# Performance work log

Measured on AMD Instinct MI355X. Metric: run time of the kernel, lower is better.

The kernel has to match this reference:

```python
import jax, jax.numpy as jnp
import numpy as np

B, P, K = 32, 1024, 16  # clouds, points per cloud, neighbors


def setup_inputs() -> dict:
    key = jax.random.key(0)
    ks = jax.random.split(key, 5)
    N, C, H, D = B * P, 64, 128, 3
    x = jax.random.normal(ks[0], (N, C), dtype=jnp.float32)
    pos = jax.random.normal(ks[1], (N, D), dtype=jnp.float32)
    batch = jnp.arange(N, dtype=jnp.int64) // P  # cloud id per node
    W_e = jax.random.normal(ks[2], (2 * C, H), dtype=jnp.float32) * 0.05
    b_e = jnp.zeros((H,), dtype=jnp.float32)
    W_sc = jax.random.normal(ks[3], (C, H), dtype=jnp.float32) * 0.05
    b_sc = jnp.zeros((H,), dtype=jnp.float32)
    return {"x": x, "pos": pos, "batch": batch,
            "W_e": W_e, "b_e": b_e, "W_sc": W_sc, "b_sc": b_sc}


def _knn_idx(posb):
    # posb: [B, P, D] -> idx [B, P, K]: K nearest neighbors (sources) per target node,
    # within each cloud, excluding self (loop=False in torch_geometric.knn_graph).
    sq = jnp.sum(posb * posb, axis=-1)                       # [B, P]
    d2 = sq[:, :, None] + sq[:, None, :] - 2.0 * jnp.einsum('bid,bjd->bij', posb, posb)
    d2 = d2 + jnp.eye(P, dtype=posb.dtype)[None] * jnp.finfo(posb.dtype).max / 2
    _, idx = jax.lax.top_k(-d2, K)                           # [B, P, K]
    return idx


def reference(x, pos, batch, W_e, b_e, W_sc, b_sc):
    C = x.shape[-1]
    xb = x.reshape(B, P, C)
    posb = pos.reshape(B, P, -1)
    idx = _knn_idx(posb)                                     # [B, P, K]
    # gather neighbor (source) features per target node
    x_j = jax.vmap(lambda xc, ic: xc[ic])(xb, idx)           # [B, P, K, C]
    x_i = xb[:, :, None, :]                                  # [B, P, 1, C]
    # EdgeConv message: nn([x_i, x_j - x_i]), here Linear + ReLU
    e = jnp.concatenate([jnp.broadcast_to(x_i, x_j.shape), x_j - x_i], axis=-1)  # [B,P,K,2C]
    msg = jax.nn.relu(jnp.einsum('bpke,eh->bpkh', e, W_e) + b_e)
    agg = jnp.max(msg, axis=2)                               # max aggregation -> [B, P, H]
    shortcut = x @ W_sc + b_sc                               # [N, H]
    out = agg.reshape(-1, agg.shape[-1]) + shortcut
    return out
```

## Files before the change

kernel.cpp:

```cpp
#include <hip/hip_runtime.h>
#include <float.h>
#include <stdint.h>

#define BATCHES 32
#define P 1024
#define KNN 16
#define C 64
#define H 128
#define N (BATCHES * P)
#define NCOLS 384
#define SPLITS 8
#define CPS 128
#define PADH 132

typedef short short8 __attribute__((ext_vector_type(8)));
typedef float floatx4 __attribute__((ext_vector_type(4)));

__device__ __forceinline__ unsigned short f2bf(float f) {
    unsigned u = __float_as_uint(f);
    unsigned r = (u + 0x7FFF + ((u >> 16) & 1)) >> 16;
    return (unsigned short)r;
}

__global__ __launch_bounds__(256) void prep_w(
    const float* __restrict__ W_e, const float* __restrict__ b_e,
    const float* __restrict__ W_sc, const float* __restrict__ b_sc,
    unsigned short* __restrict__ WT, float* __restrict__ bias)
{
    int i = blockIdx.x * 256 + threadIdx.x;
    int col = i >> 6, c = i & 63;
    float w;
    if (col < 128)      w = W_e[c * 128 + col] - W_e[(64 + c) * 128 + col];
    else if (col < 256) w = W_e[(64 + c) * 128 + (col - 128)];
    else                w = W_sc[c * 128 + (col - 256)];
    WT[col * 64 + c] = f2bf(w);
    if (c == 0) {
        bias[col] = (col < 128) ? b_e[col] : (col < 256 ? 0.0f : b_sc[col - 256]);
    }
}

struct alignas(16) F4 { float x, y, z, w; };

struct PA {
    F4    spos[P + 8];
    float lists[SPLITS][16][64];
    unsigned short offs[SPLITS][64];
    unsigned short cnts[SPLITS][64];
    float Tq[64];
};
struct PB {
    unsigned short Ubuf[64][PADH];
    unsigned short Vbuf[64][PADH];
    unsigned short Sbuf[64][PADH];
};

__global__ __launch_bounds__(512) void knn_gemm_kernel(
    const float* __restrict__ pos, const float* __restrict__ X,
    const unsigned short* __restrict__ WT, const float* __restrict__ bias,
    int* __restrict__ idx_out,
    unsigned short* __restrict__ U, unsigned short* __restrict__ V,
    unsigned short* __restrict__ S)
{
    __shared__ __align__(16) char smraw[sizeof(PA)];
    PA* A  = (PA*)smraw;
    PB* Bm = (PB*)smraw;

    int t = threadIdx.x;
    int q = t & 63, s = t >> 6;
    int blk = blockIdx.x;
    int batch = blk >> 4;
    int qblk  = blk & 15;
    int iloc  = qblk * 64 + q;

    const float* pb = pos + (size_t)batch * P * 3;
    for (int j = t; j < P; j += 512) {
        float x = pb[j * 3 + 0], y = pb[j * 3 + 1], z = pb[j * 3 + 2];
        float sq = __fadd_rn(__fadd_rn(__fmul_rn(x, x), __fmul_rn(y, y)),
                             __fmul_rn(z, z));
        A->spos[j] = F4{x, y, z, sq};
    }
    __syncthreads();

    F4 me = A->spos[iloc];
    const int j0 = s * CPS;

    float d[16];
#pragma unroll
    for (int k = 0; k < 16; ++k) d[k] = FLT_MAX;

    auto dist = [&](const F4& c, int j) -> float {
        float dot = __fadd_rn(__fadd_rn(__fmul_rn(me.x, c.x), __fmul_rn(me.y, c.y)),
                              __fmul_rn(me.z, c.z));
        float d2 = __fadd_rn(__fadd_rn(me.w, c.w), __fmul_rn(-2.0f, dot));
        return (j == iloc) ? FLT_MAX : d2;
    };
    auto insert = [&](float d2) {
#pragma unroll
        for (int k = 15; k >= 1; --k)
            d[k] = __builtin_amdgcn_fmed3f(d[k - 1], d2, d[k]);
        d[0] = fminf(d[0], d2);
    };

    {
        F4 c0 = A->spos[j0 + 0], c1 = A->spos[j0 + 1];
        F4 c2 = A->spos[j0 + 2], c3 = A->spos[j0 + 3];
#pragma unroll 2
        for (int jj = 0; jj < CPS; jj += 4) {
            F4 n0 = A->spos[j0 + jj + 4];
            F4 n1 = A->spos[j0 + jj + 5];
            F4 n2 = A->spos[j0 + jj + 6];
            F4 n3 = A->spos[j0 + jj + 7];
            insert(dist(c0, j0 + jj + 0));
            insert(dist(c1, j0 + jj + 1));
            insert(dist(c2, j0 + jj + 2));
            insert(dist(c3, j0 + jj + 3));
            c0 = n0; c1 = n1; c2 = n2; c3 = n3;
        }
    }
#pragma unroll
    for (int k = 0; k < 16; ++k) A->lists[s][k][q] = d[k];
    __syncthreads();

    if (s == 0) {
        float v0 = A->lists[0][0][q], v1 = A->lists[1][0][q];
        float v2 = A->lists[2][0][q], v3 = A->lists[3][0][q];
        float v4 = A->lists[4][0][q], v5 = A->lists[5][0][q];
        float v6 = A->lists[6][0][q], v7 = A->lists[7][0][q];
        float w0 = A->lists[0][1][q], w1 = A->lists[1][1][q];
        float w2 = A->lists[2][1][q], w3 = A->lists[3][1][q];
        float w4 = A->lists[4][1][q], w5 = A->lists[5][1][q];
        float w6 = A->lists[6][1][q], w7 = A->lists[7][1][q];
        int n0 = 0, n1 = 0, n2 = 0, n3 = 0, n4 = 0, n5 = 0, n6 = 0, n7 = 0;
        float T = 0.0f;
#pragma unroll 1
        for (int k = 0; k < 16; ++k) {
            float mn = fminf(fminf(fminf(v0, v1), fminf(v2, v3)),
                             fminf(fminf(v4, v5), fminf(v6, v7)));
            if      (v0 == mn) { n0++; v0 = w0; w0 = (n0 + 1 < 16) ? A->lists[0][n0 + 1][q] : FLT_MAX; }
            else if (v1 == mn) { n1++; v1 = w1; w1 = (n1 + 1 < 16) ? A->lists[1][n1 + 1][q] : FLT_MAX; }
            else if (v2 == mn) { n2++; v2 = w2; w2 = (n2 + 1 < 16) ? A->lists[2][n2 + 1][q] : FLT_MAX; }
            else if (v3 == mn) { n3++; v3 = w3; w3 = (n3 + 1 < 16) ? A->lists[3][n3 + 1][q] : FLT_MAX; }
            else if (v4 == mn) { n4++; v4 = w4; w4 = (n4 + 1 < 16) ? A->lists[4][n4 + 1][q] : FLT_MAX; }
            else if (v5 == mn) { n5++; v5 = w5; w5 = (n5 + 1 < 16) ? A->lists[5][n5 + 1][q] : FLT_MAX; }
            else if (v6 == mn) { n6++; v6 = w6; w6 = (n6 + 1 < 16) ? A->lists[6][n6 + 1][q] : FLT_MAX; }
            else               { n7++; v7 = w7; w7 = (n7 + 1 < 16) ? A->lists[7][n7 + 1][q] : FLT_MAX; }
            T = mn;
        }
        A->Tq[q] = T;
        int off = 0;
        A->offs[0][q] = (unsigned short)off; A->cnts[0][q] = (unsigned short)n0; off += n0;
        A->offs[1][q] = (unsigned short)off; A->cnts[1][q] = (unsigned short)n1; off += n1;
        A->offs[2][q] = (unsigned short)off; A->cnts[2][q] = (unsigned short)n2; off += n2;
        A->offs[3][q] = (unsigned short)off; A->cnts[3][q] = (unsigned short)n3; off += n3;
        A->offs[4][q] = (unsigned short)off; A->cnts[4][q] = (unsigned short)n4; off += n4;
        A->offs[5][q] = (unsigned short)off; A->cnts[5][q] = (unsigned short)n5; off += n5;
        A->offs[6][q] = (unsigned short)off; A->cnts[6][q] = (unsigned short)n6; off += n6;
        A->offs[7][q] = (unsigned short)off; A->cnts[7][q] = (unsigned short)n7;
    }
    __syncthreads();

    {
        float T  = A->Tq[q];
        int   cap = A->cnts[s][q];
        int   gb  = ((blk << 6) + q) * KNN + A->offs[s][q];
        int   base = batch * P;
        int   cnt = 0;

        F4 c0 = A->spos[j0 + 0], c1 = A->spos[j0 + 1];
        F4 c2 = A->spos[j0 + 2], c3 = A->spos[j0 + 3];
#pragma unroll 2
        for (int jj = 0; jj < CPS; jj += 4) {
            F4 n0 = A->spos[j0 + jj + 4];
            F4 n1 = A->spos[j0 + jj + 5];
            F4 n2 = A->spos[j0 + jj + 6];
            F4 n3 = A->spos[j0 + jj + 7];
#pragma unroll
            for (int u = 0; u < 4; ++u) {
                const F4& c = (u == 0) ? c0 : (u == 1) ? c1 : (u == 2) ? c2 : c3;
                int j = j0 + jj + u;
                float d2 = dist(c, j);
                if (d2 <= T && cnt < cap) {
                    idx_out[gb + cnt] = base + j;
                    cnt++;
                }
            }
            c0 = n0; c1 = n1; c2 = n2; c3 = n3;
        }
    }
    __syncthreads();

    {
        int mt = s & 3, nh = s >> 2;
        int m0 = blk * 64 + mt * 16;
        int lm = q & 15, kg = q >> 4;

        const float4* arow = (const float4*)(X + (size_t)(m0 + lm) * 64 + kg * 8);
        float4 f0 = arow[0], f1 = arow[1];
        float4 f2 = arow[8], f3 = arow[9];
        short8 a0, a1;
        a0[0] = (short)f2bf(f0.x); a0[1] = (short)f2bf(f0.y);
        a0[2] = (short)f2bf(f0.z); a0[3] = (short)f2bf(f0.w);
        a0[4] = (short)f2bf(f1.x); a0[5] = (short)f2bf(f1.y);
        a0[6] = (short)f2bf(f1.z); a0[7] = (short)f2bf(f1.w);
        a1[0] = (short)f2bf(f2.x); a1[1] = (short)f2bf(f2.y);
        a1[2] = (short)f2bf(f2.z); a1[3] = (short)f2bf(f2.w);
        a1[4] = (short)f2bf(f3.x); a1[5] = (short)f2bf(f3.y);
        a1[6] = (short)f2bf(f3.z); a1[7] = (short)f2bf(f3.w);

#pragma unroll 4
        for (int nt = nh * 12; nt < nh * 12 + 12; ++nt) {
            const short8* brow = (const short8*)(WT + (size_t)(nt * 16 + lm) * 64 + kg * 8);
            short8 b0 = brow[0];
            short8 b1 = brow[4];
            floatx4 acc = {0.0f, 0.0f, 0.0f, 0.0f};
            acc = __builtin_amdgcn_mfma_f32_16x16x32_bf16(a0, b0, acc, 0, 0, 0);
            acc = __builtin_amdgcn_mfma_f32_16x16x32_bf16(a1, b1, acc, 0, 0, 0);

            int col = nt * 16 + lm;
            float bv = bias[col];
#pragma unroll
            for (int r = 0; r < 4; ++r) {
                int row = mt * 16 + kg * 4 + r;
                unsigned short val = f2bf(acc[r] + bv);
                if (col < 128)      Bm->Ubuf[row][col] = val;
                else if (col < 256) Bm->Vbuf[row][col - 128] = val;
                else                Bm->Sbuf[row][col - 256] = val;
            }
        }
    }
    __syncthreads();

    {
        uint2* Ug = (uint2*)U + (size_t)blk * 2048;
        uint2* Vg = (uint2*)V + (size_t)blk * 2048;
        uint2* Sg = (uint2*)S + (size_t)blk * 2048;
#pragma unroll
        for (int i = t; i < 2048; i += 512) {
            int row = i >> 5, off = (i & 31) * 4;
            Ug[i] = *(const uint2*)&Bm->Ubuf[row][off];
            Vg[i] = *(const uint2*)&Bm->Vbuf[row][off];
            Sg[i] = *(const uint2*)&Bm->Sbuf[row][off];
        }
    }
}

__global__ __launch_bounds__(256) void final_kernel(
    const int* __restrict__ idx, const unsigned short* __restrict__ U,
    const unsigned short* __restrict__ V, const unsigned short* __restrict__ S,
    float* __restrict__ out)
{
    int t = threadIdx.x;
    __shared__ int nbr[8][KNN];
    if (t < 128) ((int*)nbr)[t] = idx[(size_t)blockIdx.x * 128 + t];
    __syncthreads();

    int w = t >> 6, l = t & 63;
    int half = l >> 5, c4 = l & 31;
    int pl = w * 2 + half;
    size_t p = (size_t)blockIdx.x * 8 + pl;

    uint2 uu = ((const uint2*)(U + p * H))[c4];
    uint2 ss = ((const uint2*)(S + p * H))[c4];

    float m0 = -FLT_MAX, m1 = -FLT_MAX, m2 = -FLT_MAX, m3 = -FLT_MAX;
#pragma unroll
    for (int k = 0; k < KNN; ++k) {
        int row = nbr[pl][k];
        uint2 vv = *(const uint2*)(V + (size_t)row * H + c4 * 4);
        m0 = fmaxf(m0, __uint_as_float(vv.x << 16));
        m1 = fmaxf(m1, __uint_as_float(vv.x & 0xFFFF0000u));
        m2 = fmaxf(m2, __uint_as_float(vv.y << 16));
        m3 = fmaxf(m3, __uint_as_float(vv.y & 0xFFFF0000u));
    }

    float4 o;
    o.x = fmaxf(__uint_as_float(uu.x << 16)          + m0, 0.0f) + __uint_as_float(ss.x << 16);
    o.y = fmaxf(__uint_as_float(uu.x & 0xFFFF0000u)  + m1, 0.0f) + __uint_as_float(ss.x & 0xFFFF0000u);
    o.z = fmaxf(__uint_as_float(uu.y << 16)          + m2, 0.0f) + __uint_as_float(ss.y << 16);
    o.w = fmaxf(__uint_as_float(uu.y & 0xFFFF0000u)  + m3, 0.0f) + __uint_as_float(ss.y & 0xFFFF0000u);
    ((float4*)(out + p * H))[c4] = o;
}

extern "C" void kernel_launch(void* const* d_in, const int* in_sizes, int n_in,
                              void* d_out, int out_size, void* d_ws, size_t ws_size,
                              hipStream_t stream)
{
    const float* x    = (const float*)d_in[0];
    const float* pos  = (const float*)d_in[1];
    const float* W_e  = (const float*)d_in[3];
    const float* b_e  = (const float*)d_in[4];
    const float* W_sc = (const float*)d_in[5];
    const float* b_sc = (const float*)d_in[6];
    float* out = (float*)d_out;

    char* ws = (char*)d_ws;
    const size_t OFF_IDX  = 0;
    const size_t OFF_U    = 2ull << 20;
    const size_t OFF_V    = OFF_U + (8ull << 20);
    const size_t OFF_S    = OFF_V + (8ull << 20);
    const size_t OFF_WT   = OFF_S + (8ull << 20);
    const size_t OFF_BIAS = OFF_WT + 49152;

    int*            idx  = (int*)(ws + OFF_IDX);
    unsigned short* U    = (unsigned short*)(ws + OFF_U);
    unsigned short* V    = (unsigned short*)(ws + OFF_V);
    unsigned short* S    = (unsigned short*)(ws + OFF_S);
    unsigned short* WT   = (unsigned short*)(ws + OFF_WT);
    float*          bias = (float*)(ws + OFF_BIAS);

    prep_w<<<(NCOLS * C) / 256, 256, 0, stream>>>(W_e, b_e, W_sc, b_sc, WT, bias);
    knn_gemm_kernel<<<512, 512, 0, stream>>>(pos, x, WT, bias, idx, U, V, S);
    final_kernel<<<N / 8, 256, 0, stream>>>(idx, U, V, S, out);
}
```

Baseline: 144.2 us.

## Precompute packed pos+norm in prep kernel; read candidates from global instead of LDS

The per-point packing of positions and squared norms moves into the prep kernel, which writes a float4 array to workspace. The kNN kernel no longer stages all 1024 points of its cloud into shared memory. It reads candidate positions directly from global memory, where they are wave-uniform and so can become scalar loads thanks to readfirstlane on the split index. This cuts the LDS footprint and removes a sync, which may raise occupancy, but it adds a global read path and an extra workspace buffer.

Measured after the change: 147.4 us. 2.2% more time.

```diff
diff --git a/kernel.cpp b/kernel.cpp
--- a/kernel.cpp
+++ b/kernel.cpp
@@ -22,27 +22,36 @@
     return (unsigned short)r;
 }
 
-__global__ __launch_bounds__(256) void prep_w(
+struct alignas(16) F4 { float x, y, z, w; };
+
+__global__ __launch_bounds__(256) void prep_kernel(
     const float* __restrict__ W_e, const float* __restrict__ b_e,
     const float* __restrict__ W_sc, const float* __restrict__ b_sc,
-    unsigned short* __restrict__ WT, float* __restrict__ bias)
-{
-    int i = blockIdx.x * 256 + threadIdx.x;
-    int col = i >> 6, c = i & 63;
-    float w;
-    if (col < 128)      w = W_e[c * 128 + col] - W_e[(64 + c) * 128 + col];
-    else if (col < 256) w = W_e[(64 + c) * 128 + (col - 128)];
-    else                w = W_sc[c * 128 + (col - 256)];
-    WT[col * 64 + c] = f2bf(w);
-    if (c == 0) {
-        bias[col] = (col < 128) ? b_e[col] : (col < 256 ? 0.0f : b_sc[col - 256]);
-    }
-}
-
-struct alignas(16) F4 { float x, y, z, w; };
+    const float* __restrict__ pos,
+    unsigned short* __restrict__ WT, float* __restrict__ bias,
+    F4* __restrict__ posq)
+{
+    int b = blockIdx.x;
+    if (b < 96) {
+        int i = b * 256 + threadIdx.x;
+        int col = i >> 6, c = i & 63;
+        float w;
+        if (col < 128)      w = W_e[c * 128 + col] - W_e[(64 + c) * 128 + col];
+        else if (col < 256) w = W_e[(64 + c) * 128 + (col - 128)];
+        else                w = W_sc[c * 128 + (col - 256)];
+        WT[col * 64 + c] = f2bf(w);
+        if (c == 0)
+            bias[col] = (col < 128) ? b_e[col] : (col < 256 ? 0.0f : b_sc[col - 256]);
+    } else {
+        int i = (b - 96) * 256 + threadIdx.x;
+        float x = pos[i * 3 + 0], y = pos[i * 3 + 1], z = pos[i * 3 + 2];
+        float sq = __fadd_rn(__fadd_rn(__fmul_rn(x, x), __fmul_rn(y, y)),
+                             __fmul_rn(z, z));
+        posq[i] = F4{x, y, z, sq};
+    }
+}
 
 struct PA {
-    F4    spos[P + 8];
     float lists[SPLITS][16][64];
     unsigned short offs[SPLITS][64];
     unsigned short cnts[SPLITS][64];
@@ -55,67 +64,48 @@
 };
 
 __global__ __launch_bounds__(512) void knn_gemm_kernel(
-    const float* __restrict__ pos, const float* __restrict__ X,
+    const F4* __restrict__ posq, const float* __restrict__ X,
     const unsigned short* __restrict__ WT, const float* __restrict__ bias,
     int* __restrict__ idx_out,
     unsigned short* __restrict__ U, unsigned short* __restrict__ V,
     unsigned short* __restrict__ S)
 {
-    __shared__ __align__(16) char smraw[sizeof(PA)];
+    __shared__ __align__(16) char smraw[sizeof(PB)];
     PA* A  = (PA*)smraw;
     PB* Bm = (PB*)smraw;
 
     int t = threadIdx.x;
-    int q = t & 63, s = t >> 6;
+    int q = t & 63;
+    int s = __builtin_amdgcn_readfirstlane(t >> 6);
     int blk = blockIdx.x;
     int batch = blk >> 4;
     int qblk  = blk & 15;
     int iloc  = qblk * 64 + q;
 
-    const float* pb = pos + (size_t)batch * P * 3;
-    for (int j = t; j < P; j += 512) {
-        float x = pb[j * 3 + 0], y = pb[j * 3 + 1], z = pb[j * 3 + 2];
-        float sq = __fadd_rn(__fadd_rn(__fmul_rn(x, x), __fmul_rn(y, y)),
-                             __fmul_rn(z, z));
-        A->spos[j] = F4{x, y, z, sq};
-    }
-    __syncthreads();
-
-    F4 me = A->spos[iloc];
+    const F4* __restrict__ pbq = posq + (size_t)batch * P;
     const int j0 = s * CPS;
-
-    float d[16];
-#pragma unroll
-    for (int k = 0; k < 16; ++k) d[k] = FLT_MAX;
-
-    auto dist = [&](const F4& c, int j) -> float {
+    const F4* __restrict__ pcand = pbq + j0;
+
+    F4 me = pbq[iloc];
+
+    auto dist = [&](F4 c, int j) -> float {
         float dot = __fadd_rn(__fadd_rn(__fmul_rn(me.x, c.x), __fmul_rn(me.y, c.y)),
                               __fmul_rn(me.z, c.z));
         float d2 = __fadd_rn(__fadd_rn(me.w, c.w), __fmul_rn(-2.0f, dot));
         return (j == iloc) ? FLT_MAX : d2;
     };
-    auto insert = [&](float d2) {
+
+    float d[16];
+#pragma unroll
+    for (int k = 0; k < 16; ++k) d[k] = FLT_MAX;
+
+#pragma unroll 8
+    for (int jj = 0; jj < CPS; ++jj) {
+        float d2 = dist(pcand[jj], j0 + jj);
 #pragma unroll
         for (int k = 15; k >= 1; --k)
             d[k] = __builtin_amdgcn_fmed3f(d[k - 1], d2, d[k]);
         d[0] = fminf(d[0], d2);
-    };
-
-    {
-        F4 c0 = A->spos[j0 + 0], c1 = A->spos[j0 + 1];
-        F4 c2 = A->spos[j0 + 2], c3 = A->spos[j0 + 3];
-#pragma unroll 2
-        for (int jj = 0; jj < CPS; jj += 4) {
-            F4 n0 = A->spos[j0 + jj + 4];
-            F4 n1 = A->spos[j0 + jj + 5];
-            F4 n2 = A->spos[j0 + jj + 6];
-            F4 n3 = A->spos[j0 + jj + 7];
-            insert(dist(c0, j0 + jj + 0));
-            insert(dist(c1, j0 + jj + 1));
-            insert(dist(c2, j0 + jj + 2));
-            insert(dist(c3, j0 + jj + 3));
-            c0 = n0; c1 = n1; c2 = n2; c3 = n3;
-        }
     }
 #pragma unroll
     for (int k = 0; k < 16; ++k) A->lists[s][k][q] = d[k];
@@ -160,31 +150,18 @@
     __syncthreads();
 
     {
-        float T  = A->Tq[q];
+        float T   = A->Tq[q];
         int   cap = A->cnts[s][q];
         int   gb  = ((blk << 6) + q) * KNN + A->offs[s][q];
         int   base = batch * P;
         int   cnt = 0;
-
-        F4 c0 = A->spos[j0 + 0], c1 = A->spos[j0 + 1];
-        F4 c2 = A->spos[j0 + 2], c3 = A->spos[j0 + 3];
-#pragma unroll 2
-        for (int jj = 0; jj < CPS; jj += 4) {
-            F4 n0 = A->spos[j0 + jj + 4];
-            F4 n1 = A->spos[j0 + jj + 5];
-            F4 n2 = A->spos[j0 + jj + 6];
-            F4 n3 = A->spos[j0 + jj + 7];
-#pragma unroll
-            for (int u = 0; u < 4; ++u) {
-                const F4& c = (u == 0) ? c0 : (u == 1) ? c1 : (u == 2) ? c2 : c3;
-                int j = j0 + jj + u;
-                float d2 = dist(c, j);
-                if (d2 <= T && cnt < cap) {
-                    idx_out[gb + cnt] = base + j;
-                    cnt++;
-                }
+#pragma unroll 4
+        for (int jj = 0; jj < CPS; ++jj) {
+            float d2 = dist(pcand[jj], j0 + jj);
+            if (d2 <= T && cnt < cap) {
+                idx_out[gb + cnt] = base + j0 + jj;
+                cnt++;
             }
-            c0 = n0; c1 = n1; c2 = n2; c3 = n3;
         }
     }
     __syncthreads();
@@ -298,17 +275,19 @@
     const size_t OFF_U    = 2ull << 20;
     const size_t OFF_V    = OFF_U + (8ull << 20);
     const size_t OFF_S    = OFF_V + (8ull << 20);
-    const size_t OFF_WT   = OFF_S + (8ull << 20);
+    const size_t OFF_PQ   = OFF_S + (8ull << 20);
+    const size_t OFF_WT   = OFF_PQ + (512ull << 10);
     const size_t OFF_BIAS = OFF_WT + 49152;
 
     int*            idx  = (int*)(ws + OFF_IDX);
     unsigned short* U    = (unsigned short*)(ws + OFF_U);
     unsigned short* V    = (unsigned short*)(ws + OFF_V);
     unsigned short* S    = (unsigned short*)(ws + OFF_S);
+    F4*             posq = (F4*)(ws + OFF_PQ);
     unsigned short* WT   = (unsigned short*)(ws + OFF_WT);
     float*          bias = (float*)(ws + OFF_BIAS);
 
-    prep_w<<<(NCOLS * C) / 256, 256, 0, stream>>>(W_e, b_e, W_sc, b_sc, WT, bias);
-    knn_gemm_kernel<<<512, 512, 0, stream>>>(pos, x, WT, bias, idx, U, V, S);
+    prep_kernel<<<224, 256, 0, stream>>>(W_e, b_e, W_sc, b_sc, pos, WT, bias, posq);
+    knn_gemm_kernel<<<512, 512, 0, stream>>>(posq, x, WT, bias, idx, U, V, S);
     final_kernel<<<N / 8, 256, 0, stream>>>(idx, U, V, S, out);
 }
```
